# Optimization experiments

Hardware: AMD Instinct MI355X
Metric: run time of the kernel (lower is better)

The kernel has to match this reference:

```python
import jax, jax.numpy as jnp
import numpy as np

B, S, C = 2, 4096, 512
H = 8            # num heads
D = C // H       # head dim = 64


def setup_inputs() -> dict:
    key = jax.random.key(0)
    ks = jax.random.split(key, 5)
    s = 0.02
    return {
        "hidden_states": jax.random.normal(ks[0], (B, S, C), dtype=jnp.float32),
        "Wq": jax.random.normal(ks[1], (C, C), dtype=jnp.float32) * s,
        "Wk": jax.random.normal(ks[2], (C, C), dtype=jnp.float32) * s,
        "Wv": jax.random.normal(ks[3], (C, C), dtype=jnp.float32) * s,
        "Wo": jax.random.normal(ks[4], (C, C), dtype=jnp.float32) * s,
        "bo": jnp.zeros((C,), dtype=jnp.float32),
    }


def reference(hidden_states, Wq, Wk, Wv, Wo, bo):
    # Self-attention path of AttnProcessor (encoder_hidden_states=None,
    # no norms, no mask, residual_connection=False, rescale=1.0).
    b, s, c = hidden_states.shape
    scale = jnp.float32(D) ** -0.5
    # QKV projections (Linear, no bias as in diffusers defaults)
    q = hidden_states @ Wq.T   # [b,s,c]
    k = hidden_states @ Wk.T
    v = hidden_states @ Wv.T
    # head_to_batch_dim: [b,s,c] -> [b,s,h,d]
    q = q.reshape(b, s, H, D)
    k = k.reshape(b, s, H, D)
    v = v.reshape(b, s, H, D)
    # get_attention_scores: scaled QK^T + softmax (full O(S^2) matrix, as in source)
    scores = jnp.einsum("bqhd,bkhd->bhqk", q, k) * scale   # [b,h,s,s]
    probs = jax.nn.softmax(scores, axis=-1)
    # bmm with V, batch_to_head_dim
    out = jnp.einsum("bhqk,bkhd->bqhd", probs, v).reshape(b, s, c)
    # to_out[0] (Linear with bias); to_out[1] is Dropout (identity at eval)
    out = out @ Wo.T + bo
    return out
```

## Files before the change

### kernel.cpp

```cpp
#include <hip/hip_runtime.h>
#include <hip/hip_bf16.h>

#define BB 2
#define SS 4096
#define CC 512
#define HH 8
#define DD 64
#define MM (BB*SS)

typedef __bf16 bf16;
typedef __attribute__((ext_vector_type(8))) __bf16 bf16x8;
typedef __attribute__((ext_vector_type(4))) __bf16 bf16x4;
typedef __attribute__((ext_vector_type(4))) float f32x4;

#define LP 72
#define QSCALE 0.18033688f

__device__ __forceinline__ float exp2_fast(float x) {
  float r;
  asm("v_exp_f32 %0, %1" : "=v"(r) : "v"(x));
  return r;
}

__device__ __forceinline__ bf16x8 cvt8(const float4 a, const float4 b) {
  bf16x8 r;
  r[0]=(bf16)a.x; r[1]=(bf16)a.y; r[2]=(bf16)a.z; r[3]=(bf16)a.w;
  r[4]=(bf16)b.x; r[5]=(bf16)b.y; r[6]=(bf16)b.z; r[7]=(bf16)b.w;
  return r;
}

__global__ __launch_bounds__(256) void cvt_f32_bf16(
    const float* __restrict__ src, bf16* __restrict__ dst)
{
  size_t e = ((size_t)blockIdx.x * 256 + threadIdx.x) * 8;
  float4 a = ((const float4*)(src + e))[0];
  float4 b = ((const float4*)(src + e))[1];
  *(bf16x8*)(dst + e) = cvt8(a, b);
}

__global__ __launch_bounds__(256) void cvt_w(
    const float* __restrict__ Wq, const float* __restrict__ Wk,
    const float* __restrict__ Wv, bf16* __restrict__ Wb)
{
  size_t e = ((size_t)blockIdx.x * 256 + threadIdx.x) * 8;
  const int tens = (int)(e >> 18);
  const float* src = ((tens == 0) ? Wq : (tens == 1) ? Wk : Wv) + (e & 262143);
  const float sc = (tens == 0) ? QSCALE : 1.f;
  float4 a = ((const float4*)src)[0];
  float4 b = ((const float4*)src)[1];
  bf16x8 r;
  r[0]=(bf16)(a.x*sc); r[1]=(bf16)(a.y*sc); r[2]=(bf16)(a.z*sc); r[3]=(bf16)(a.w*sc);
  r[4]=(bf16)(b.x*sc); r[5]=(bf16)(b.y*sc); r[6]=(bf16)(b.z*sc); r[7]=(bf16)(b.w*sc);
  *(bf16x8*)(Wb + e) = r;
}

__global__ __launch_bounds__(256) void qkv_gemm(
    const bf16* __restrict__ Xb, const bf16* __restrict__ Wb,
    bf16* __restrict__ qp, bf16* __restrict__ kp, bf16* __restrict__ vtp)
{
  __shared__ bf16 Aa[64*LP];
  __shared__ bf16 Ab[64*LP];
  __shared__ bf16 Ba[64*LP];
  __shared__ bf16 Bb[64*LP];
  const int m0  = blockIdx.x * 128;
  const int nf0 = blockIdx.y * 128;
  const int tens = nf0 >> 9;
  const int n0 = nf0 & 511;

  const int t = threadIdx.x;
  const int w = t >> 6;
  const int lane = t & 63;
  const int l15 = lane & 15;
  const int quad = lane >> 4;
  const int srow = t >> 2;
  const int scol = (t & 3) << 4;

  f32x4 acc[2][2][4];
  #pragma unroll
  for (int mi = 0; mi < 2; ++mi)
    #pragma unroll
    for (int ni = 0; ni < 2; ++ni)
      #pragma unroll
      for (int nt = 0; nt < 4; ++nt)
        #pragma unroll
        for (int r = 0; r < 4; ++r) acc[mi][ni][nt][r] = 0.f;

  for (int k0 = 0; k0 < CC; k0 += 64) {
    __syncthreads();
    {
      const bf16* sa = Xb + (size_t)(m0 + srow) * CC + k0 + scol;
      *(bf16x8*)&Aa[srow*LP + scol]     = ((const bf16x8*)sa)[0];
      *(bf16x8*)&Aa[srow*LP + scol + 8] = ((const bf16x8*)sa)[1];
      const bf16* sb = Xb + (size_t)(m0 + 64 + srow) * CC + k0 + scol;
      *(bf16x8*)&Ab[srow*LP + scol]     = ((const bf16x8*)sb)[0];
      *(bf16x8*)&Ab[srow*LP + scol + 8] = ((const bf16x8*)sb)[1];
      const bf16* s1 = Wb + (size_t)(nf0 + srow) * CC + k0 + scol;
      *(bf16x8*)&Ba[srow*LP + scol]     = ((const bf16x8*)s1)[0];
      *(bf16x8*)&Ba[srow*LP + scol + 8] = ((const bf16x8*)s1)[1];
      const bf16* s2 = Wb + (size_t)(nf0 + 64 + srow) * CC + k0 + scol;
      *(bf16x8*)&Bb[srow*LP + scol]     = ((const bf16x8*)s2)[0];
      *(bf16x8*)&Bb[srow*LP + scol + 8] = ((const bf16x8*)s2)[1];
    }
    __syncthreads();
    #pragma unroll
    for (int c = 0; c < 2; ++c) {
      bf16x8 afa = *(const bf16x8*)&Aa[(w*16 + l15)*LP + c*32 + quad*8];
      bf16x8 afb = *(const bf16x8*)&Ab[(w*16 + l15)*LP + c*32 + quad*8];
      #pragma unroll
      for (int nt = 0; nt < 4; ++nt) {
        bf16x8 ba = *(const bf16x8*)&Ba[(nt*16 + l15)*LP + c*32 + quad*8];
        bf16x8 bb = *(const bf16x8*)&Bb[(nt*16 + l15)*LP + c*32 + quad*8];
        acc[0][0][nt] = __builtin_amdgcn_mfma_f32_16x16x32_bf16(afa, ba, acc[0][0][nt], 0, 0, 0);
        acc[1][0][nt] = __builtin_amdgcn_mfma_f32_16x16x32_bf16(afb, ba, acc[1][0][nt], 0, 0, 0);
        acc[0][1][nt] = __builtin_amdgcn_mfma_f32_16x16x32_bf16(afa, bb, acc[0][1][nt], 0, 0, 0);
        acc[1][1][nt] = __builtin_amdgcn_mfma_f32_16x16x32_bf16(afb, bb, acc[1][1][nt], 0, 0, 0);
      }
    }
  }

  bf16* plane = (tens == 0) ? qp : ((tens == 1) ? kp : vtp);
  const int c8 = (t & 7) * 8;

  auto epi = [&](const f32x4* as, int mt0, int nb) {
    const int b = mt0 >> 12, s0g = mt0 & 4095;
    const int h = nb >> 6;
    __syncthreads();
    if (tens < 2) {
      #pragma unroll
      for (int nt = 0; nt < 4; ++nt)
        #pragma unroll
        for (int r = 0; r < 4; ++r)
          Aa[(w*16 + quad*4 + r)*LP + nt*16 + l15] = (bf16)as[nt][r];
    } else {
      #pragma unroll
      for (int nt = 0; nt < 4; ++nt)
        #pragma unroll
        for (int r = 0; r < 4; ++r)
          Aa[(nt*16 + l15)*LP + w*16 + quad*4 + r] = (bf16)as[nt][r];
    }
    __syncthreads();
    #pragma unroll
    for (int i = 0; i < 2; ++i) {
      const int row = (t >> 3) + 32*i;
      bf16x8 v = *(const bf16x8*)&Aa[row*LP + c8];
      if (tens < 2) {
        *(bf16x8*)&plane[((size_t)((b*HH + h)*SS) + s0g + row)*DD + c8] = v;
      } else {
        *(bf16x8*)&plane[((size_t)((b*HH + h)*DD) + row)*SS + s0g + c8] = v;
      }
    }
  };

  epi(acc[0][0], m0,      n0);
  epi(acc[1][0], m0 + 64, n0);
  epi(acc[0][1], m0,      n0 + 64);
  epi(acc[1][1], m0 + 64, n0 + 64);
}

__global__ __launch_bounds__(256) void attn_fa(
    const bf16* __restrict__ qpl, const bf16* __restrict__ kpl,
    const bf16* __restrict__ vtpl, bf16* __restrict__ aout)
{
  __shared__ bf16 Kt[2][64*LP];
  __shared__ bf16 Vt[2][64*LP];

  const int t = threadIdx.x;
  const int w = t >> 6;
  const int lane = t & 63;
  const int l15 = lane & 15;
  const int quad = lane >> 4;

  const int lin = blockIdx.x;
  const int bh = lin & 15;
  const int q0 = (lin >> 4) * 128;
  const size_t plane = (size_t)SS * DD;
  const bf16* Qp = qpl + (size_t)bh * plane;
  const bf16* Kp = kpl + (size_t)bh * plane;
  const bf16* Vg = vtpl + (size_t)bh * plane;

  bf16x8 qf[2][2];
  #pragma unroll
  for (int wq = 0; wq < 2; ++wq) {
    const bf16* qr = Qp + (size_t)(q0 + w*32 + wq*16 + l15) * DD + quad*8;
    qf[wq][0] = *(const bf16x8*)qr;
    qf[wq][1] = *(const bf16x8*)(qr + 32);
  }

  f32x4 o[2][4];
  float rs[2] = {0.f, 0.f};
  #pragma unroll
  for (int wq = 0; wq < 2; ++wq)
    #pragma unroll
    for (int nt = 0; nt < 4; ++nt)
      #pragma unroll
      for (int r = 0; r < 4; ++r) o[wq][nt][r] = 0.f;

  const int r0 = t >> 3;
  const int c0 = (t & 7) * 8;
  const int koff = (c0 >> 5)*32 + ((c0 >> 3) & 3)*4;

  bf16x8 ka0, ka1;
  bf16x4 v00, v01, v10, v11;
  {
    ka0 = *(const bf16x8*)&Kp[(size_t)r0*DD + c0];
    ka1 = *(const bf16x8*)&Kp[(size_t)(r0 + 32)*DD + c0];
    v00 = *(const bf16x4*)&Vg[(size_t)r0*SS + koff];
    v01 = *(const bf16x4*)&Vg[(size_t)r0*SS + koff + 16];
    v10 = *(const bf16x4*)&Vg[(size_t)(r0+32)*SS + koff];
    v11 = *(const bf16x4*)&Vg[(size_t)(r0+32)*SS + koff + 16];
    *(bf16x8*)&Kt[0][r0*LP + c0]      = ka0;
    *(bf16x8*)&Kt[0][(r0+32)*LP + c0] = ka1;
    bf16x8 vv;
    vv[0]=v00[0]; vv[1]=v00[1]; vv[2]=v00[2]; vv[3]=v00[3];
    vv[4]=v01[0]; vv[5]=v01[1]; vv[6]=v01[2]; vv[7]=v01[3];
    *(bf16x8*)&Vt[0][r0*LP + c0] = vv;
    vv[0]=v10[0]; vv[1]=v10[1]; vv[2]=v10[2]; vv[3]=v10[3];
    vv[4]=v11[0]; vv[5]=v11[1]; vv[6]=v11[2]; vv[7]=v11[3];
    *(bf16x8*)&Vt[0][(r0+32)*LP + c0] = vv;
  }
  __syncthreads();

  for (int it = 0; it < SS/64; ++it) {
    const int cur = it & 1;
    if (it < SS/64 - 1) {
      const int kb = (it + 1) * 64;
      ka0 = *(const bf16x8*)&Kp[(size_t)(kb + r0)*DD + c0];
      ka1 = *(const bf16x8*)&Kp[(size_t)(kb + r0 + 32)*DD + c0];
      v00 = *(const bf16x4*)&Vg[(size_t)r0*SS + kb + koff];
      v01 = *(const bf16x4*)&Vg[(size_t)r0*SS + kb + koff + 16];
      v10 = *(const bf16x4*)&Vg[(size_t)(r0+32)*SS + kb + koff];
      v11 = *(const bf16x4*)&Vg[(size_t)(r0+32)*SS + kb + koff + 16];
    }

    f32x4 st[2][4];
    #pragma unroll
    for (int nt = 0; nt < 4; ++nt) {
      bf16x8 kf0 = *(const bf16x8*)&Kt[cur][(nt*16 + l15)*LP + quad*8];
      bf16x8 kf1 = *(const bf16x8*)&Kt[cur][(nt*16 + l15)*LP + 32 + quad*8];
      #pragma unroll
      for (int wq = 0; wq < 2; ++wq) {
        f32x4 z; z[0]=z[1]=z[2]=z[3]=0.f;
        z = __builtin_amdgcn_mfma_f32_16x16x32_bf16(kf0, qf[wq][0], z, 0, 0, 0);
        z = __builtin_amdgcn_mfma_f32_16x16x32_bf16(kf1, qf[wq][1], z, 0, 0, 0);
        st[wq][nt] = z;
      }
    }

    bf16x8 pb[2][2];
    #pragma unroll
    for (int wq = 0; wq < 2; ++wq) {
      float acc_s = 0.f;
      #pragma unroll
      for (int nt = 0; nt < 4; ++nt)
        #pragma unroll
        for (int r = 0; r < 4; ++r) {
          float pv = exp2_fast(st[wq][nt][r]);
          acc_s += pv;
          pb[wq][nt >> 1][(nt & 1)*4 + r] = (bf16)pv;
        }
      rs[wq] += acc_s;
    }

    #pragma unroll
    for (int kbh = 0; kbh < 2; ++kbh) {
      #pragma unroll
      for (int nt = 0; nt < 4; ++nt) {
        bf16x8 vf = *(const bf16x8*)&Vt[cur][(nt*16 + l15)*LP + kbh*32 + quad*8];
        #pragma unroll
        for (int wq = 0; wq < 2; ++wq)
          o[wq][nt] = __builtin_amdgcn_mfma_f32_16x16x32_bf16(vf, pb[wq][kbh], o[wq][nt], 0, 0, 0);
      }
    }

    if (it < SS/64 - 1) {
      const int nxt = cur ^ 1;
      *(bf16x8*)&Kt[nxt][r0*LP + c0]      = ka0;
      *(bf16x8*)&Kt[nxt][(r0+32)*LP + c0] = ka1;
      bf16x8 vv;
      vv[0]=v00[0]; vv[1]=v00[1]; vv[2]=v00[2]; vv[3]=v00[3];
      vv[4]=v01[0]; vv[5]=v01[1]; vv[6]=v01[2]; vv[7]=v01[3];
      *(bf16x8*)&Vt[nxt][r0*LP + c0] = vv;
      vv[0]=v10[0]; vv[1]=v10[1]; vv[2]=v10[2]; vv[3]=v10[3];
      vv[4]=v11[0]; vv[5]=v11[1]; vv[6]=v11[2]; vv[7]=v11[3];
      *(bf16x8*)&Vt[nxt][(r0+32)*LP + c0] = vv;
      __syncthreads();
    }
  }

  const int b = bh >> 3, h = bh & 7;
  #pragma unroll
  for (int wq = 0; wq < 2; ++wq) {
    float s = rs[wq];
    s += __shfl_xor(s, 16);
    s += __shfl_xor(s, 32);
    const float inv = 1.f / s;
    const size_t row = (size_t)(b*SS + q0 + w*32 + wq*16 + l15) * CC + h*DD;
    #pragma unroll
    for (int nt = 0; nt < 4; ++nt) {
      bf16x4 ov;
      #pragma unroll
      for (int r = 0; r < 4; ++r) ov[r] = (bf16)(o[wq][nt][r] * inv);
      *(bf16x4*)&aout[row + nt*16 + quad*4] = ov;
    }
  }
}

__global__ __launch_bounds__(256) void out_gemm(
    const bf16* __restrict__ A, const bf16* __restrict__ Wob,
    const float* __restrict__ bo, float* __restrict__ out)
{
  __shared__ bf16 Aa[64*LP];
  __shared__ bf16 Ab[64*LP];
  __shared__ bf16 Bt[64*LP];
  const int m0 = blockIdx.x * 128;
  const int n0 = blockIdx.y * 64;

  const int t = threadIdx.x;
  const int w = t >> 6;
  const int lane = t & 63;
  const int l15 = lane & 15;
  const int quad = lane >> 4;
  const int srow = t >> 2;
  const int scol = (t & 3) << 4;

  f32x4 aca[4], acb[4];
  #pragma unroll
  for (int i = 0; i < 4; ++i)
    #pragma unroll
    for (int j = 0; j < 4; ++j) { aca[i][j] = 0.f; acb[i][j] = 0.f; }

  for (int k0 = 0; k0 < CC; k0 += 64) {
    __syncthreads();
    {
      const bf16* sa = A + (size_t)(m0 + srow) * CC + k0 + scol;
      *(bf16x8*)&Aa[srow*LP + scol]     = ((const bf16x8*)sa)[0];
      *(bf16x8*)&Aa[srow*LP + scol + 8] = ((const bf16x8*)sa)[1];
      const bf16* sb = A + (size_t)(m0 + 64 + srow) * CC + k0 + scol;
      *(bf16x8*)&Ab[srow*LP + scol]     = ((const bf16x8*)sb)[0];
      *(bf16x8*)&Ab[srow*LP + scol + 8] = ((const bf16x8*)sb)[1];
      const bf16* s1 = Wob + (size_t)(n0 + srow) * CC + k0 + scol;
      *(bf16x8*)&Bt[srow*LP + scol]     = ((const bf16x8*)s1)[0];
      *(bf16x8*)&Bt[srow*LP + scol + 8] = ((const bf16x8*)s1)[1];
    }
    __syncthreads();
    #pragma unroll
    for (int c = 0; c < 2; ++c) {
      bf16x8 afa = *(const bf16x8*)&Aa[(w*16 + l15)*LP + c*32 + quad*8];
      bf16x8 afb = *(const bf16x8*)&Ab[(w*16 + l15)*LP + c*32 + quad*8];
      #pragma unroll
      for (int nt = 0; nt < 4; ++nt) {
        bf16x8 bfr = *(const bf16x8*)&Bt[(nt*16 + l15)*LP + c*32 + quad*8];
        aca[nt] = __builtin_amdgcn_mfma_f32_16x16x32_bf16(afa, bfr, aca[nt], 0, 0, 0);
        acb[nt] = __builtin_amdgcn_mfma_f32_16x16x32_bf16(afb, bfr, acb[nt], 0, 0, 0);
      }
    }
  }

  #pragma unroll
  for (int nt = 0; nt < 4; ++nt) {
    const int ng = n0 + nt*16 + l15;
    const float bias = bo[ng];
    #pragma unroll
    for (int r = 0; r < 4; ++r) {
      const int mga = m0 + w*16 + quad*4 + r;
      out[(size_t)mga*CC + ng] = aca[nt][r] + bias;
      const int mgb = m0 + 64 + w*16 + quad*4 + r;
      out[(size_t)mgb*CC + ng] = acb[nt][r] + bias;
    }
  }
}

extern "C" void kernel_launch(void* const* d_in, const int* in_sizes, int n_in,
                              void* d_out, int out_size, void* d_ws, size_t ws_size,
                              hipStream_t stream) {
  const float* hs = (const float*)d_in[0];
  const float* Wq = (const float*)d_in[1];
  const float* Wk = (const float*)d_in[2];
  const float* Wv = (const float*)d_in[3];
  const float* Wo = (const float*)d_in[4];
  const float* bo = (const float*)d_in[5];
  float* out = (float*)d_out;

  const size_t PE = (size_t)BB*HH*SS*DD;
  bf16* ws   = (bf16*)d_ws;
  bf16* qp   = ws;
  bf16* kp   = ws + PE;
  bf16* vtp  = ws + 2*PE;
  bf16* Xb   = ws + 3*PE;
  bf16* aout = ws + 3*PE;
  bf16* Wob  = qp;
  bf16* Wb   = ws + 4*PE;

  cvt_f32_bf16<<<dim3(2048),      256, 0, stream>>>(hs, Xb);
  cvt_w       <<<dim3(384),       256, 0, stream>>>(Wq, Wk, Wv, Wb);
  qkv_gemm<<<dim3(MM/128, 12),    256, 0, stream>>>(Xb, Wb, qp, kp, vtp);
  attn_fa <<<dim3(512),           256, 0, stream>>>(qp, kp, vtp, aout);
  cvt_f32_bf16<<<dim3(128),       256, 0, stream>>>(Wo, Wob);
  out_gemm<<<dim3(MM/128, CC/64), 256, 0, stream>>>(aout, Wob, bo, out);
}
```

Baseline: 200.0 us.

## Split attention block across 8 waves with one 16-row Q tile each

The attention kernel moves from 4 waves per block, each owning two 16-row query tiles, to 8 waves per block, each owning one. The cooperative K/V tile load is spread over 512 threads, so each thread loads half as much, and launch bounds request 4 blocks per CU. This halves per-wave accumulator registers and raises wave count for latency hiding, at the cost of each K/V LDS fragment read now feeding only one MFMA pair instead of two. The inline-asm exp2 is also replaced by the compiler builtin.

```diff
diff --git a/kernel.cpp b/kernel.cpp
--- a/kernel.cpp
+++ b/kernel.cpp
@@ -15,12 +15,6 @@
 
 #define LP 72
 #define QSCALE 0.18033688f
-
-__device__ __forceinline__ float exp2_fast(float x) {
-  float r;
-  asm("v_exp_f32 %0, %1" : "=v"(r) : "v"(x));
-  return r;
-}
 
 __device__ __forceinline__ bf16x8 cvt8(const float4 a, const float4 b) {
   bf16x8 r;
@@ -157,7 +151,7 @@
   epi(acc[1][1], m0 + 64, n0 + 64);
 }
 
-__global__ __launch_bounds__(256) void attn_fa(
+__global__ __launch_bounds__(512, 4) void attn_fa(
     const bf16* __restrict__ qpl, const bf16* __restrict__ kpl,
     const bf16* __restrict__ vtpl, bf16* __restrict__ aout)
 {
@@ -178,45 +172,35 @@
   const bf16* Kp = kpl + (size_t)bh * plane;
   const bf16* Vg = vtpl + (size_t)bh * plane;
 
-  bf16x8 qf[2][2];
+  bf16x8 qf[2];
+  {
+    const bf16* qr = Qp + (size_t)(q0 + w*16 + l15) * DD + quad*8;
+    qf[0] = *(const bf16x8*)qr;
+    qf[1] = *(const bf16x8*)(qr + 32);
+  }
+
+  f32x4 o[4];
+  float rs = 0.f;
   #pragma unroll
-  for (int wq = 0; wq < 2; ++wq) {
-    const bf16* qr = Qp + (size_t)(q0 + w*32 + wq*16 + l15) * DD + quad*8;
-    qf[wq][0] = *(const bf16x8*)qr;
-    qf[wq][1] = *(const bf16x8*)(qr + 32);
-  }
-
-  f32x4 o[2][4];
-  float rs[2] = {0.f, 0.f};
-  #pragma unroll
-  for (int wq = 0; wq < 2; ++wq)
-    #pragma unroll
-    for (int nt = 0; nt < 4; ++nt)
-      #pragma unroll
-      for (int r = 0; r < 4; ++r) o[wq][nt][r] = 0.f;
+  for (int nt = 0; nt < 4; ++nt)
+    #pragma unroll
+    for (int r = 0; r < 4; ++r) o[nt][r] = 0.f;
 
   const int r0 = t >> 3;
   const int c0 = (t & 7) * 8;
   const int koff = (c0 >> 5)*32 + ((c0 >> 3) & 3)*4;
 
-  bf16x8 ka0, ka1;
-  bf16x4 v00, v01, v10, v11;
+  bf16x8 ka;
+  bf16x4 v0, v1;
   {
-    ka0 = *(const bf16x8*)&Kp[(size_t)r0*DD + c0];
-    ka1 = *(const bf16x8*)&Kp[(size_t)(r0 + 32)*DD + c0];
-    v00 = *(const bf16x4*)&Vg[(size_t)r0*SS + koff];
-    v01 = *(const bf16x4*)&Vg[(size_t)r0*SS + koff + 16];
-    v10 = *(const bf16x4*)&Vg[(size_t)(r0+32)*SS + koff];
-    v11 = *(const bf16x4*)&Vg[(size_t)(r0+32)*SS + koff + 16];
-    *(bf16x8*)&Kt[0][r0*LP + c0]      = ka0;
-    *(bf16x8*)&Kt[0][(r0+32)*LP + c0] = ka1;
+    ka = *(const bf16x8*)&Kp[(size_t)r0*DD + c0];
+    v0 = *(const bf16x4*)&Vg[(size_t)r0*SS + koff];
+    v1 = *(const bf16x4*)&Vg[(size_t)r0*SS + koff + 16];
+    *(bf16x8*)&Kt[0][r0*LP + c0] = ka;
     bf16x8 vv;
-    vv[0]=v00[0]; vv[1]=v00[1]; vv[2]=v00[2]; vv[3]=v00[3];
-    vv[4]=v01[0]; vv[5]=v01[1]; vv[6]=v01[2]; vv[7]=v01[3];
+    vv[0]=v0[0]; vv[1]=v0[1]; vv[2]=v0[2]; vv[3]=v0[3];
+    vv[4]=v1[0]; vv[5]=v1[1]; vv[6]=v1[2]; vv[7]=v1[3];
     *(bf16x8*)&Vt[0][r0*LP + c0] = vv;
-    vv[0]=v10[0]; vv[1]=v10[1]; vv[2]=v10[2]; vv[3]=v10[3];
-    vv[4]=v11[0]; vv[5]=v11[1]; vv[6]=v11[2]; vv[7]=v11[3];
-    *(bf16x8*)&Vt[0][(r0+32)*LP + c0] = vv;
   }
   __syncthreads();
 
@@ -224,41 +208,34 @@
     const int cur = it & 1;
     if (it < SS/64 - 1) {
       const int kb = (it + 1) * 64;
-      ka0 = *(const bf16x8*)&Kp[(size_t)(kb + r0)*DD + c0];
-      ka1 = *(const bf16x8*)&Kp[(size_t)(kb + r0 + 32)*DD + c0];
-      v00 = *(const bf16x4*)&Vg[(size_t)r0*SS + kb + koff];
-      v01 = *(const bf16x4*)&Vg[(size_t)r0*SS + kb + koff + 16];
-      v10 = *(const bf16x4*)&Vg[(size_t)(r0+32)*SS + kb + koff];
-      v11 = *(const bf16x4*)&Vg[(size_t)(r0+32)*SS + kb + koff + 16];
-    }
-
-    f32x4 st[2][4];
+      ka = *(const bf16x8*)&Kp[(size_t)(kb + r0)*DD + c0];
+      v0 = *(const bf16x4*)&Vg[(size_t)r0*SS + kb + koff];
+      v1 = *(const bf16x4*)&Vg[(size_t)r0*SS + kb + koff + 16];
+    }
+
+    f32x4 st[4];
     #pragma unroll
     for (int nt = 0; nt < 4; ++nt) {
       bf16x8 kf0 = *(const bf16x8*)&Kt[cur][(nt*16 + l15)*LP + quad*8];
       bf16x8 kf1 = *(const bf16x8*)&Kt[cur][(nt*16 + l15)*LP + 32 + quad*8];
-      #pragma unroll
-      for (int wq = 0; wq < 2; ++wq) {
-        f32x4 z; z[0]=z[1]=z[2]=z[3]=0.f;
-        z = __builtin_amdgcn_mfma_f32_16x16x32_bf16(kf0, qf[wq][0], z, 0, 0, 0);
-        z = __builtin_amdgcn_mfma_f32_16x16x32_bf16(kf1, qf[wq][1], z, 0, 0, 0);
-        st[wq][nt] = z;
-      }
-    }
-
-    bf16x8 pb[2][2];
-    #pragma unroll
-    for (int wq = 0; wq < 2; ++wq) {
+      f32x4 z; z[0]=z[1]=z[2]=z[3]=0.f;
+      z = __builtin_amdgcn_mfma_f32_16x16x32_bf16(kf0, qf[0], z, 0, 0, 0);
+      z = __builtin_amdgcn_mfma_f32_16x16x32_bf16(kf1, qf[1], z, 0, 0, 0);
+      st[nt] = z;
+    }
+
+    bf16x8 pb[2];
+    {
       float acc_s = 0.f;
       #pragma unroll
       for (int nt = 0; nt < 4; ++nt)
         #pragma unroll
         for (int r = 0; r < 4; ++r) {
-          float pv = exp2_fast(st[wq][nt][r]);
+          float pv = __builtin_amdgcn_exp2f(st[nt][r]);
           acc_s += pv;
-          pb[wq][nt >> 1][(nt & 1)*4 + r] = (bf16)pv;
+          pb[nt >> 1][(nt & 1)*4 + r] = (bf16)pv;
         }
-      rs[wq] += acc_s;
+      rs += acc_s;
     }
 
     #pragma unroll
@@ -266,40 +243,33 @@
       #pragma unroll
       for (int nt = 0; nt < 4; ++nt) {
         bf16x8 vf = *(const bf16x8*)&Vt[cur][(nt*16 + l15)*LP + kbh*32 + quad*8];
-        #pragma unroll
-        for (int wq = 0; wq < 2; ++wq)
-          o[wq][nt] = __builtin_amdgcn_mfma_f32_16x16x32_bf16(vf, pb[wq][kbh], o[wq][nt], 0, 0, 0);
+        o[nt] = __builtin_amdgcn_mfma_f32_16x16x32_bf16(vf, pb[kbh], o[nt], 0, 0, 0);
       }
     }
 
     if (it < SS/64 - 1) {
       const int nxt = cur ^ 1;
-      *(bf16x8*)&Kt[nxt][r0*LP + c0]      = ka0;
-      *(bf16x8*)&Kt[nxt][(r0+32)*LP + c0] = ka1;
+      *(bf16x8*)&Kt[nxt][r0*LP + c0] = ka;
       bf16x8 vv;
-      vv[0]=v00[0]; vv[1]=v00[1]; vv[2]=v00[2]; vv[3]=v00[3];
-      vv[4]=v01[0]; vv[5]=v01[1]; vv[6]=v01[2]; vv[7]=v01[3];
+      vv[0]=v0[0]; vv[1]=v0[1]; vv[2]=v0[2]; vv[3]=v0[3];
+      vv[4]=v1[0]; vv[5]=v1[1]; vv[6]=v1[2]; vv[7]=v1[3];
       *(bf16x8*)&Vt[nxt][r0*LP + c0] = vv;
-      vv[0]=v10[0]; vv[1]=v10[1]; vv[2]=v10[2]; vv[3]=v10[3];
-      vv[4]=v11[0]; vv[5]=v11[1]; vv[6]=v11[2]; vv[7]=v11[3];
-      *(bf16x8*)&Vt[nxt][(r0+32)*LP + c0] = vv;
       __syncthreads();
     }
   }
 
   const int b = bh >> 3, h = bh & 7;
-  #pragma unroll
-  for (int wq = 0; wq < 2; ++wq) {
-    float s = rs[wq];
+  {
+    float s = rs;
     s += __shfl_xor(s, 16);
     s += __shfl_xor(s, 32);
     const float inv = 1.f / s;
-    const size_t row = (size_t)(b*SS + q0 + w*32 + wq*16 + l15) * CC + h*DD;
+    const size_t row = (size_t)(b*SS + q0 + w*16 + l15) * CC + h*DD;
     #pragma unroll
     for (int nt = 0; nt < 4; ++nt) {
       bf16x4 ov;
       #pragma unroll
-      for (int r = 0; r < 4; ++r) ov[r] = (bf16)(o[wq][nt][r] * inv);
+      for (int r = 0; r < 4; ++r) ov[r] = (bf16)(o[nt][r] * inv);
       *(bf16x4*)&aout[row + nt*16 + quad*4] = ov;
     }
   }
@@ -394,7 +364,7 @@
   cvt_f32_bf16<<<dim3(2048),      256, 0, stream>>>(hs, Xb);
   cvt_w       <<<dim3(384),       256, 0, stream>>>(Wq, Wk, Wv, Wb);
   qkv_gemm<<<dim3(MM/128, 12),    256, 0, stream>>>(Xb, Wb, qp, kp, vtp);
-  attn_fa <<<dim3(512),           256, 0, stream>>>(qp, kp, vtp, aout);
+  attn_fa <<<dim3(512),           512, 0, stream>>>(qp, kp, vtp, aout);
   cvt_f32_bf16<<<dim3(128),       256, 0, stream>>>(Wo, Wob);
   out_gemm<<<dim3(MM/128, CC/64), 256, 0, stream>>>(aout, Wob, bo, out);
 }
```

New measurement: 192.0 us. -4.0%, faster.

## Split attention KV range across two wave groups per block with LDS reduction

Applied to the files above, without the earlier changes.

The attention kernel now launches 512 threads per block. Two groups of four waves each process half of the key sequence for the same 128 query rows, using separate double-buffered LDS tiles. The partial outputs and row sums are then combined through LDS before normalisation. This can be done without rescaling because the softmax here skips max subtraction. The aim is to double the waves per block and hide latency, since only 512 blocks are launched. The costs are twice the LDS per block, an extra reduction step, and a changed global load pattern for the V tiles.

```diff
diff --git a/kernel.cpp b/kernel.cpp
--- a/kernel.cpp
+++ b/kernel.cpp
@@ -15,12 +15,6 @@
 
 #define LP 72
 #define QSCALE 0.18033688f
-
-__device__ __forceinline__ float exp2_fast(float x) {
-  float r;
-  asm("v_exp_f32 %0, %1" : "=v"(r) : "v"(x));
-  return r;
-}
 
 __device__ __forceinline__ bf16x8 cvt8(const float4 a, const float4 b) {
   bf16x8 r;
@@ -157,15 +151,16 @@
   epi(acc[1][1], m0 + 64, n0 + 64);
 }
 
-__global__ __launch_bounds__(256) void attn_fa(
+__global__ __launch_bounds__(512, 4) void attn_fa(
     const bf16* __restrict__ qpl, const bf16* __restrict__ kpl,
     const bf16* __restrict__ vtpl, bf16* __restrict__ aout)
 {
-  __shared__ bf16 Kt[2][64*LP];
-  __shared__ bf16 Vt[2][64*LP];
+  __shared__ __align__(16) bf16 smem[2 * 4 * 64 * LP];
 
   const int t = threadIdx.x;
   const int w = t >> 6;
+  const int g = w >> 2;
+  const int wl = w & 3;
   const int lane = t & 63;
   const int l15 = lane & 15;
   const int quad = lane >> 4;
@@ -178,10 +173,13 @@
   const bf16* Kp = kpl + (size_t)bh * plane;
   const bf16* Vg = vtpl + (size_t)bh * plane;
 
+  bf16* Ktg = smem + g * (4*64*LP);
+  bf16* Vtg = Ktg + 2*64*LP;
+
   bf16x8 qf[2][2];
   #pragma unroll
   for (int wq = 0; wq < 2; ++wq) {
-    const bf16* qr = Qp + (size_t)(q0 + w*32 + wq*16 + l15) * DD + quad*8;
+    const bf16* qr = Qp + (size_t)(q0 + wl*32 + wq*16 + l15) * DD + quad*8;
     qf[wq][0] = *(const bf16x8*)qr;
     qf[wq][1] = *(const bf16x8*)(qr + 32);
   }
@@ -195,48 +193,48 @@
       #pragma unroll
       for (int r = 0; r < 4; ++r) o[wq][nt][r] = 0.f;
 
-  const int r0 = t >> 3;
-  const int c0 = (t & 7) * 8;
-  const int koff = (c0 >> 5)*32 + ((c0 >> 3) & 3)*4;
-
-  bf16x8 ka0, ka1;
-  bf16x4 v00, v01, v10, v11;
+  const int t8  = t & 255;
+  const int r0s = t8 >> 2;
+  const int cs  = (t8 & 3) << 4;
+  const int K0  = ((t8 & 1) << 3) + (((t8 >> 1) & 1) << 5);
+  const int kbase = g << 11;
+
+  bf16x8 ka0, ka1, va, vb;
   {
-    ka0 = *(const bf16x8*)&Kp[(size_t)r0*DD + c0];
-    ka1 = *(const bf16x8*)&Kp[(size_t)(r0 + 32)*DD + c0];
-    v00 = *(const bf16x4*)&Vg[(size_t)r0*SS + koff];
-    v01 = *(const bf16x4*)&Vg[(size_t)r0*SS + koff + 16];
-    v10 = *(const bf16x4*)&Vg[(size_t)(r0+32)*SS + koff];
-    v11 = *(const bf16x4*)&Vg[(size_t)(r0+32)*SS + koff + 16];
-    *(bf16x8*)&Kt[0][r0*LP + c0]      = ka0;
-    *(bf16x8*)&Kt[0][(r0+32)*LP + c0] = ka1;
+    ka0 = *(const bf16x8*)&Kp[(size_t)(kbase + r0s)*DD + cs];
+    ka1 = *(const bf16x8*)&Kp[(size_t)(kbase + r0s)*DD + cs + 8];
+    va  = *(const bf16x8*)&Vg[(size_t)r0s*SS + kbase + K0];
+    vb  = *(const bf16x8*)&Vg[(size_t)r0s*SS + kbase + K0 + 16];
+    *(bf16x8*)&Ktg[r0s*LP + cs]     = ka0;
+    *(bf16x8*)&Ktg[r0s*LP + cs + 8] = ka1;
     bf16x8 vv;
-    vv[0]=v00[0]; vv[1]=v00[1]; vv[2]=v00[2]; vv[3]=v00[3];
-    vv[4]=v01[0]; vv[5]=v01[1]; vv[6]=v01[2]; vv[7]=v01[3];
-    *(bf16x8*)&Vt[0][r0*LP + c0] = vv;
-    vv[0]=v10[0]; vv[1]=v10[1]; vv[2]=v10[2]; vv[3]=v10[3];
-    vv[4]=v11[0]; vv[5]=v11[1]; vv[6]=v11[2]; vv[7]=v11[3];
-    *(bf16x8*)&Vt[0][(r0+32)*LP + c0] = vv;
+    vv[0]=va[0]; vv[1]=va[1]; vv[2]=va[2]; vv[3]=va[3];
+    vv[4]=vb[0]; vv[5]=vb[1]; vv[6]=vb[2]; vv[7]=vb[3];
+    *(bf16x8*)&Vtg[r0s*LP + cs] = vv;
+    vv[0]=va[4]; vv[1]=va[5]; vv[2]=va[6]; vv[3]=va[7];
+    vv[4]=vb[4]; vv[5]=vb[5]; vv[6]=vb[6]; vv[7]=vb[7];
+    *(bf16x8*)&Vtg[r0s*LP + cs + 8] = vv;
   }
   __syncthreads();
 
-  for (int it = 0; it < SS/64; ++it) {
+  for (int it = 0; it < 32; ++it) {
     const int cur = it & 1;
-    if (it < SS/64 - 1) {
-      const int kb = (it + 1) * 64;
-      ka0 = *(const bf16x8*)&Kp[(size_t)(kb + r0)*DD + c0];
-      ka1 = *(const bf16x8*)&Kp[(size_t)(kb + r0 + 32)*DD + c0];
-      v00 = *(const bf16x4*)&Vg[(size_t)r0*SS + kb + koff];
-      v01 = *(const bf16x4*)&Vg[(size_t)r0*SS + kb + koff + 16];
-      v10 = *(const bf16x4*)&Vg[(size_t)(r0+32)*SS + kb + koff];
-      v11 = *(const bf16x4*)&Vg[(size_t)(r0+32)*SS + kb + koff + 16];
-    }
+    if (it < 31) {
+      const int kb = kbase + (it + 1) * 64;
+      ka0 = *(const bf16x8*)&Kp[(size_t)(kb + r0s)*DD + cs];
+      ka1 = *(const bf16x8*)&Kp[(size_t)(kb + r0s)*DD + cs + 8];
+      va  = *(const bf16x8*)&Vg[(size_t)r0s*SS + kb + K0];
+      vb  = *(const bf16x8*)&Vg[(size_t)r0s*SS + kb + K0 + 16];
+    }
+
+    const bf16* Ktc = Ktg + cur*(64*LP);
+    const bf16* Vtc = Vtg + cur*(64*LP);
 
     f32x4 st[2][4];
     #pragma unroll
     for (int nt = 0; nt < 4; ++nt) {
-      bf16x8 kf0 = *(const bf16x8*)&Kt[cur][(nt*16 + l15)*LP + quad*8];
-      bf16x8 kf1 = *(const bf16x8*)&Kt[cur][(nt*16 + l15)*LP + 32 + quad*8];
+      bf16x8 kf0 = *(const bf16x8*)&Ktc[(nt*16 + l15)*LP + quad*8];
+      bf16x8 kf1 = *(const bf16x8*)&Ktc[(nt*16 + l15)*LP + 32 + quad*8];
       #pragma unroll
       for (int wq = 0; wq < 2; ++wq) {
         f32x4 z; z[0]=z[1]=z[2]=z[3]=0.f;
@@ -254,7 +252,7 @@
       for (int nt = 0; nt < 4; ++nt)
         #pragma unroll
         for (int r = 0; r < 4; ++r) {
-          float pv = exp2_fast(st[wq][nt][r]);
+          float pv = __builtin_amdgcn_exp2f(st[wq][nt][r]);
           acc_s += pv;
           pb[wq][nt >> 1][(nt & 1)*4 + r] = (bf16)pv;
         }
@@ -265,42 +263,70 @@
     for (int kbh = 0; kbh < 2; ++kbh) {
       #pragma unroll
       for (int nt = 0; nt < 4; ++nt) {
-        bf16x8 vf = *(const bf16x8*)&Vt[cur][(nt*16 + l15)*LP + kbh*32 + quad*8];
+        bf16x8 vf = *(const bf16x8*)&Vtc[(nt*16 + l15)*LP + kbh*32 + quad*8];
         #pragma unroll
         for (int wq = 0; wq < 2; ++wq)
           o[wq][nt] = __builtin_amdgcn_mfma_f32_16x16x32_bf16(vf, pb[wq][kbh], o[wq][nt], 0, 0, 0);
       }
     }
 
-    if (it < SS/64 - 1) {
+    if (it < 31) {
       const int nxt = cur ^ 1;
-      *(bf16x8*)&Kt[nxt][r0*LP + c0]      = ka0;
-      *(bf16x8*)&Kt[nxt][(r0+32)*LP + c0] = ka1;
+      bf16* Ktn = Ktg + nxt*(64*LP);
+      bf16* Vtn = Vtg + nxt*(64*LP);
+      *(bf16x8*)&Ktn[r0s*LP + cs]     = ka0;
+      *(bf16x8*)&Ktn[r0s*LP + cs + 8] = ka1;
       bf16x8 vv;
-      vv[0]=v00[0]; vv[1]=v00[1]; vv[2]=v00[2]; vv[3]=v00[3];
-      vv[4]=v01[0]; vv[5]=v01[1]; vv[6]=v01[2]; vv[7]=v01[3];
-      *(bf16x8*)&Vt[nxt][r0*LP + c0] = vv;
-      vv[0]=v10[0]; vv[1]=v10[1]; vv[2]=v10[2]; vv[3]=v10[3];
-      vv[4]=v11[0]; vv[5]=v11[1]; vv[6]=v11[2]; vv[7]=v11[3];
-      *(bf16x8*)&Vt[nxt][(r0+32)*LP + c0] = vv;
+      vv[0]=va[0]; vv[1]=va[1]; vv[2]=va[2]; vv[3]=va[3];
+      vv[4]=vb[0]; vv[5]=vb[1]; vv[6]=vb[2]; vv[7]=vb[3];
+      *(bf16x8*)&Vtn[r0s*LP + cs] = vv;
+      vv[0]=va[4]; vv[1]=va[5]; vv[2]=va[6]; vv[3]=va[7];
+      vv[4]=vb[4]; vv[5]=vb[5]; vv[6]=vb[6]; vv[7]=vb[7];
+      *(bf16x8*)&Vtn[r0s*LP + cs + 8] = vv;
       __syncthreads();
     }
   }
 
-  const int b = bh >> 3, h = bh & 7;
-  #pragma unroll
-  for (int wq = 0; wq < 2; ++wq) {
-    float s = rs[wq];
-    s += __shfl_xor(s, 16);
-    s += __shfl_xor(s, 32);
-    const float inv = 1.f / s;
-    const size_t row = (size_t)(b*SS + q0 + w*32 + wq*16 + l15) * CC + h*DD;
-    #pragma unroll
-    for (int nt = 0; nt < 4; ++nt) {
-      bf16x4 ov;
-      #pragma unroll
-      for (int r = 0; r < 4; ++r) ov[r] = (bf16)(o[wq][nt][r] * inv);
-      *(bf16x4*)&aout[row + nt*16 + quad*4] = ov;
+  __syncthreads();
+  float* stash = (float*)smem;
+  const int sidx = (wl*64 + lane) * 36;
+  if (g == 1) {
+    #pragma unroll
+    for (int wq = 0; wq < 2; ++wq)
+      #pragma unroll
+      for (int nt = 0; nt < 4; ++nt)
+        *(f32x4*)&stash[sidx + (wq*4 + nt)*4] = o[wq][nt];
+    stash[sidx + 32] = rs[0];
+    stash[sidx + 33] = rs[1];
+  }
+  __syncthreads();
+  if (g == 0) {
+    #pragma unroll
+    for (int wq = 0; wq < 2; ++wq)
+      #pragma unroll
+      for (int nt = 0; nt < 4; ++nt) {
+        f32x4 p = *(const f32x4*)&stash[sidx + (wq*4 + nt)*4];
+        #pragma unroll
+        for (int r = 0; r < 4; ++r) o[wq][nt][r] += p[r];
+      }
+    rs[0] += stash[sidx + 32];
+    rs[1] += stash[sidx + 33];
+
+    const int b = bh >> 3, h = bh & 7;
+    #pragma unroll
+    for (int wq = 0; wq < 2; ++wq) {
+      float s = rs[wq];
+      s += __shfl_xor(s, 16);
+      s += __shfl_xor(s, 32);
+      const float inv = 1.f / s;
+      const size_t row = (size_t)(b*SS + q0 + wl*32 + wq*16 + l15) * CC + h*DD;
+      #pragma unroll
+      for (int nt = 0; nt < 4; ++nt) {
+        bf16x4 ov;
+        #pragma unroll
+        for (int r = 0; r < 4; ++r) ov[r] = (bf16)(o[wq][nt][r] * inv);
+        *(bf16x4*)&aout[row + nt*16 + quad*4] = ov;
+      }
     }
   }
 }
@@ -394,7 +420,7 @@
   cvt_f32_bf16<<<dim3(2048),      256, 0, stream>>>(hs, Xb);
   cvt_w       <<<dim3(384),       256, 0, stream>>>(Wq, Wk, Wv, Wb);
   qkv_gemm<<<dim3(MM/128, 12),    256, 0, stream>>>(Xb, Wb, qp, kp, vtp);
-  attn_fa <<<dim3(512),           256, 0, stream>>>(qp, kp, vtp, aout);
+  attn_fa <<<dim3(512),           512, 0, stream>>>(qp, kp, vtp, aout);
   cvt_f32_bf16<<<dim3(128),       256, 0, stream>>>(Wo, Wob);
   out_gemm<<<dim3(MM/128, CC/64), 256, 0, stream>>>(aout, Wob, bo, out);
 }
```

Measured after the change: 186.7 us. 6.6% less time.
